# Performance work log

Measured on AMD Instinct MI355X. Metric: run time of the kernel, lower is better.

## Reference

```python
import jax, jax.numpy as jnp
import numpy as np

N = 100000
E = 1600000
G = 2048          # number of graphs in the batch
HEADS = 4
HID = 16          # per-head channels
IN_CH = 128
D = HEADS * HID   # 64, concat output width per layer
NEG_SLOPE = 0.2


def _gat_layer(x, src, dst, W, a_src, a_dst, bias):
    # x: [N, Fin], W: [Fin, H*C], a_src/a_dst: [H, C], bias: [H*C]
    h = (x @ W).reshape(N, HEADS, HID)                      # [N, H, C]
    al_s = jnp.einsum('nhc,hc->nh', h, a_src)               # [N, H]
    al_d = jnp.einsum('nhc,hc->nh', h, a_dst)               # [N, H]
    e = jax.nn.leaky_relu(al_s[src] + al_d[dst], NEG_SLOPE) # [E+N, H]
    # segment softmax over incoming edges of each destination node
    m = jax.ops.segment_max(e, dst, num_segments=N)         # [N, H]
    e = jnp.exp(e - m[dst])
    s = jax.ops.segment_sum(e, dst, num_segments=N)
    alpha = e / (s[dst] + 1e-16)                            # [E+N, H]
    msg = h[src] * alpha[..., None]                         # [E+N, H, C]
    out = jax.ops.segment_sum(msg, dst, num_segments=N)     # [N, H, C]
    return out.reshape(N, D) + bias


def setup_inputs() -> dict:
    key = jax.random.key(0)
    ks = jax.random.split(key, 16)
    x = jax.random.normal(ks[0], (N, IN_CH), dtype=jnp.float32)
    edge_index = jax.random.randint(ks[1], (2, E), 0, N, dtype=jnp.int64)
    batch = jnp.sort(jax.random.randint(ks[2], (N,), 0, G, dtype=jnp.int64))
    inp = {'x': x, 'edge_index': edge_index, 'batch': batch}
    fins = [IN_CH, D, D]
    for i, fin in enumerate(fins):
        kk = jax.random.split(ks[3 + i], 4)
        sc = 1.0 / np.sqrt(fin)
        inp[f'W{i}'] = jax.random.normal(kk[0], (fin, D), dtype=jnp.float32) * sc
        inp[f'as{i}'] = jax.random.normal(kk[1], (HEADS, HID), dtype=jnp.float32) * 0.1
        inp[f'ad{i}'] = jax.random.normal(kk[2], (HEADS, HID), dtype=jnp.float32) * 0.1
        inp[f'b{i}'] = jnp.zeros((D,), dtype=jnp.float32)
    inp['head_w'] = jax.random.normal(ks[10], (1, D), dtype=jnp.float32) * (1.0 / np.sqrt(D))
    inp['head_b'] = jnp.zeros((1,), dtype=jnp.float32)
    return inp


def reference(x, edge_index, batch,
              W0, as0, ad0, b0,
              W1, as1, ad1, b1,
              W2, as2, ad2, b2,
              head_w, head_b):
    # PyG GATConv adds self-loops by default
    loops = jnp.arange(N, dtype=edge_index.dtype)
    src = jnp.concatenate([edge_index[0], loops])
    dst = jnp.concatenate([edge_index[1], loops])
    layers = [(W0, as0, ad0, b0), (W1, as1, ad1, b1), (W2, as2, ad2, b2)]
    h = x.astype(jnp.float32)
    for (W, a_s, a_d, b) in layers:
        h = _gat_layer(h, src, dst, W, a_s, a_d, b)
        h = jax.nn.relu(h)  # dropout p=0.0 -> identity
    pooled = jax.ops.segment_sum(h, batch, num_segments=G)  # [G, D]
    out = pooled @ head_w.T + head_b                         # [G, 1]
    return out.reshape(-1)                                   # out_dim == 1 -> flatten
```

## Files before the change

### kernel.cpp

```cpp
#include <hip/hip_runtime.h>
#include <hip/hip_bf16.h>
#include <hip/hip_fp16.h>
#include <cstdint>
#include <cstddef>

#define NN 100000
#define EE 1600000
#define GG 2048

constexpr int NB_SCAN = (NN + 255) / 256;

typedef __attribute__((ext_vector_type(4))) _Float16 half4v;

__device__ __forceinline__ float lrelu(float v) { return v > 0.f ? v : 0.2f * v; }

__global__ void k_count(const int* __restrict__ ei, int* __restrict__ deg) {
    int i = blockIdx.x * blockDim.x + threadIdx.x;
    if (i >= EE + NN) return;
    int d = (i < EE) ? ei[EE + i] : (i - EE);
    atomicAdd(&deg[d], 1);
}

__global__ void k_scan1(const int* __restrict__ deg, int* __restrict__ offs,
                        int* __restrict__ bsums) {
    __shared__ int tmp[256];
    int tid = threadIdx.x;
    int i = blockIdx.x * 256 + tid;
    int v = (i < NN) ? deg[i] : 0;
    tmp[tid] = v; __syncthreads();
    for (int off = 1; off < 256; off <<= 1) {
        int t = (tid >= off) ? tmp[tid - off] : 0;
        __syncthreads();
        tmp[tid] += t;
        __syncthreads();
    }
    if (i < NN) offs[i] = tmp[tid] - v;
    if (tid == 255) bsums[blockIdx.x] = tmp[255];
}

__global__ void k_scan2(int* __restrict__ bsums) {
    __shared__ int tmp[512];
    int tid = threadIdx.x;
    int v = (tid < NB_SCAN) ? bsums[tid] : 0;
    tmp[tid] = v; __syncthreads();
    for (int off = 1; off < 512; off <<= 1) {
        int t = (tid >= off) ? tmp[tid - off] : 0;
        __syncthreads();
        tmp[tid] += t;
        __syncthreads();
    }
    if (tid < NB_SCAN) bsums[tid] = tmp[tid] - v;
}

__global__ void k_scan3(int* __restrict__ offs, const int* __restrict__ bsums) {
    int i = blockIdx.x * 256 + threadIdx.x;
    if (i < NN) offs[i] += bsums[blockIdx.x];
}

__global__ void k_scatter(const int* __restrict__ ei, const int* __restrict__ offs,
                          int* __restrict__ cursor, int* __restrict__ col) {
    int i = blockIdx.x * blockDim.x + threadIdx.x;
    if (i >= EE + NN) return;
    int s, d;
    if (i < EE) { s = ei[i]; d = ei[EE + i]; } else { s = d = i - EE; }
    int pos = offs[d] + atomicAdd(&cursor[d], 1);
    col[pos] = s;
}

__global__ __launch_bounds__(256) void k_gemm(const float* __restrict__ X,
                                              const float* __restrict__ W,
                                              const float* __restrict__ asrc,
                                              const float* __restrict__ adst,
                                              _Float16* __restrict__ Hh,
                                              float* __restrict__ als,
                                              float* __restrict__ ald, int fin) {
    __shared__ float xs[16 * 128];
    int j  = threadIdx.x & 63;
    int ty = threadIdx.x >> 6;
    int row0 = blockIdx.x * 16;
    int f4 = fin >> 2;
    int lg = (fin == 128) ? 5 : 4;
    const float4* X4 = (const float4*)X;
    int tot4 = 16 * f4;
    for (int idx = threadIdx.x; idx < tot4; idx += 256) {
        int r = idx >> lg, k4 = idx & (f4 - 1);
        ((float4*)xs)[idx] = X4[(size_t)(row0 + r) * f4 + k4];
    }
    __syncthreads();
    const float* x0 = xs + (ty * 4 + 0) * fin;
    const float* x1 = xs + (ty * 4 + 1) * fin;
    const float* x2 = xs + (ty * 4 + 2) * fin;
    const float* x3 = xs + (ty * 4 + 3) * fin;
    float a0 = 0.f, a1 = 0.f, a2 = 0.f, a3 = 0.f;
    for (int k = 0; k < fin; k++) {
        float w = W[k * 64 + j];
        a0 += x0[k] * w; a1 += x1[k] * w; a2 += x2[k] * w; a3 += x3[k] * w;
    }
    int row = row0 + ty * 4;
    Hh[(size_t)(row + 0) * 64 + j] = (_Float16)a0;
    Hh[(size_t)(row + 1) * 64 + j] = (_Float16)a1;
    Hh[(size_t)(row + 2) * 64 + j] = (_Float16)a2;
    Hh[(size_t)(row + 3) * 64 + j] = (_Float16)a3;
    float asj = asrc[j], adj = adst[j];
    float accs[4] = {a0, a1, a2, a3};
#pragma unroll
    for (int r = 0; r < 4; r++) {
        float vs = accs[r] * asj;
        float vd = accs[r] * adj;
#pragma unroll
        for (int off = 8; off > 0; off >>= 1) {
            vs += __shfl_xor(vs, off, 64);
            vd += __shfl_xor(vd, off, 64);
        }
        if ((j & 15) == 0) {
            int h = j >> 4;
            als[(size_t)(row + r) * 4 + h] = vs;
            ald[(size_t)(row + r) * 4 + h] = vd;
        }
    }
}

#define LWPITCH 260
__global__ __launch_bounds__(256) void k_agg(
    const _Float16* __restrict__ Hh, const float* __restrict__ als,
    const float* __restrict__ ald, const int* __restrict__ offs,
    const int* __restrict__ deg, const int* __restrict__ col,
    const float* __restrict__ bias, float* __restrict__ Hout,
    const int* __restrict__ batch, const float* __restrict__ hw,
    float* __restrict__ out, int last) {
    __shared__ float lws[16 * LWPITCH];
    __shared__ int   lsi[16][64];
    int tid = threadIdx.x;
    int g = tid >> 4;
    int l = tid & 15;
    int n = blockIdx.x * 16 + g;
    int start = offs[n];
    int len = deg[n];
    float4 ad4 = ((const float4*)ald)[n];
    int hsel = l >> 2;
    const half4v* Hp = (const half4v*)Hh + l;
    float* lw = lws + g * LWPITCH;
    bool fast = (len <= 64);
    float inv = 1.f;

    if (fast) {
        float ev[4][4];
        int   si[4];
        bool  vld[4];
        float m0 = -1e30f, m1 = -1e30f, m2 = -1e30f, m3 = -1e30f;
#pragma unroll
        for (int it = 0; it < 4; it++) {
            int e = l + it * 16;
            vld[it] = (e < len);
            int s = vld[it] ? col[start + e] : 0;
            si[it] = s;
            float4 a = ((const float4*)als)[s];
            ev[it][0] = lrelu(a.x + ad4.x); ev[it][1] = lrelu(a.y + ad4.y);
            ev[it][2] = lrelu(a.z + ad4.z); ev[it][3] = lrelu(a.w + ad4.w);
            if (vld[it]) {
                m0 = fmaxf(m0, ev[it][0]); m1 = fmaxf(m1, ev[it][1]);
                m2 = fmaxf(m2, ev[it][2]); m3 = fmaxf(m3, ev[it][3]);
            }
        }
#pragma unroll
        for (int off = 8; off > 0; off >>= 1) {
            m0 = fmaxf(m0, __shfl_xor(m0, off, 16));
            m1 = fmaxf(m1, __shfl_xor(m1, off, 16));
            m2 = fmaxf(m2, __shfl_xor(m2, off, 16));
            m3 = fmaxf(m3, __shfl_xor(m3, off, 16));
        }
        float s0 = 0.f, s1 = 0.f, s2 = 0.f, s3 = 0.f;
#pragma unroll
        for (int it = 0; it < 4; it++) {
            int e = l + it * 16;
            float w0 = vld[it] ? __expf(ev[it][0] - m0) : 0.f;
            float w1 = vld[it] ? __expf(ev[it][1] - m1) : 0.f;
            float w2 = vld[it] ? __expf(ev[it][2] - m2) : 0.f;
            float w3 = vld[it] ? __expf(ev[it][3] - m3) : 0.f;
            s0 += w0; s1 += w1; s2 += w2; s3 += w3;
            ((float4*)(lw + e * 4))[0] = make_float4(w0, w1, w2, w3);
            lsi[g][e] = vld[it] ? si[it] : 0;
        }
#pragma unroll
        for (int off = 8; off > 0; off >>= 1) {
            s0 += __shfl_xor(s0, off, 16); s1 += __shfl_xor(s1, off, 16);
            s2 += __shfl_xor(s2, off, 16); s3 += __shfl_xor(s3, off, 16);
        }
        float smh = hsel == 0 ? s0 : hsel == 1 ? s1 : hsel == 2 ? s2 : s3;
        inv = 1.f / (smh + 1e-16f);
    }

    __syncthreads();

    float4 acc = {0.f, 0.f, 0.f, 0.f};
    if (fast) {
        int e = 0;
        for (; e + 4 <= len; e += 4) {
            int sa = lsi[g][e], sb = lsi[g][e + 1], sc = lsi[g][e + 2], sd = lsi[g][e + 3];
            float wa = lw[(e + 0) * 4 + hsel];
            float wb = lw[(e + 1) * 4 + hsel];
            float wc = lw[(e + 2) * 4 + hsel];
            float wd = lw[(e + 3) * 4 + hsel];
            half4v ha = Hp[(size_t)sa * 16];
            half4v hb = Hp[(size_t)sb * 16];
            half4v hc = Hp[(size_t)sc * 16];
            half4v hd = Hp[(size_t)sd * 16];
            acc.x += wa * (float)ha.x + wb * (float)hb.x + wc * (float)hc.x + wd * (float)hd.x;
            acc.y += wa * (float)ha.y + wb * (float)hb.y + wc * (float)hc.y + wd * (float)hd.y;
            acc.z += wa * (float)ha.z + wb * (float)hb.z + wc * (float)hc.z + wd * (float)hd.z;
            acc.w += wa * (float)ha.w + wb * (float)hb.w + wc * (float)hc.w + wd * (float)hd.w;
        }
        for (; e < len; e++) {
            int sa = lsi[g][e];
            float wa = lw[e * 4 + hsel];
            half4v ha = Hp[(size_t)sa * 16];
            acc.x += wa * (float)ha.x; acc.y += wa * (float)ha.y;
            acc.z += wa * (float)ha.z; acc.w += wa * (float)ha.w;
        }
    } else {
        float m0 = -1e30f, m1 = -1e30f, m2 = -1e30f, m3 = -1e30f;
        for (int e = l; e < len; e += 16) {
            int s = col[start + e];
            float4 a = ((const float4*)als)[s];
            m0 = fmaxf(m0, lrelu(a.x + ad4.x)); m1 = fmaxf(m1, lrelu(a.y + ad4.y));
            m2 = fmaxf(m2, lrelu(a.z + ad4.z)); m3 = fmaxf(m3, lrelu(a.w + ad4.w));
        }
#pragma unroll
        for (int off = 8; off > 0; off >>= 1) {
            m0 = fmaxf(m0, __shfl_xor(m0, off, 16));
            m1 = fmaxf(m1, __shfl_xor(m1, off, 16));
            m2 = fmaxf(m2, __shfl_xor(m2, off, 16));
            m3 = fmaxf(m3, __shfl_xor(m3, off, 16));
        }
        float s0 = 0.f, s1 = 0.f, s2 = 0.f, s3 = 0.f;
        for (int e = l; e < len; e += 16) {
            int s = col[start + e];
            float4 a = ((const float4*)als)[s];
            s0 += __expf(lrelu(a.x + ad4.x) - m0); s1 += __expf(lrelu(a.y + ad4.y) - m1);
            s2 += __expf(lrelu(a.z + ad4.z) - m2); s3 += __expf(lrelu(a.w + ad4.w) - m3);
        }
#pragma unroll
        for (int off = 8; off > 0; off >>= 1) {
            s0 += __shfl_xor(s0, off, 16); s1 += __shfl_xor(s1, off, 16);
            s2 += __shfl_xor(s2, off, 16); s3 += __shfl_xor(s3, off, 16);
        }
        float mh = hsel == 0 ? m0 : hsel == 1 ? m1 : hsel == 2 ? m2 : m3;
        float sh = hsel == 0 ? s0 : hsel == 1 ? s1 : hsel == 2 ? s2 : s3;
        float ih = 1.f / (sh + 1e-16f);
        float ah = hsel == 0 ? ad4.x : hsel == 1 ? ad4.y : hsel == 2 ? ad4.z : ad4.w;
        for (int e = 0; e < len; e++) {
            int s = col[start + e];
            float alpha = __expf(lrelu(als[(size_t)s * 4 + hsel] + ah) - mh) * ih;
            half4v ha = Hp[(size_t)s * 16];
            acc.x += alpha * (float)ha.x; acc.y += alpha * (float)ha.y;
            acc.z += alpha * (float)ha.z; acc.w += alpha * (float)ha.w;
        }
        inv = 1.f;
    }

    float4 b4 = ((const float4*)bias)[l];
    float4 o4;
    o4.x = fmaxf(acc.x * inv + b4.x, 0.f);
    o4.y = fmaxf(acc.y * inv + b4.y, 0.f);
    o4.z = fmaxf(acc.z * inv + b4.z, 0.f);
    o4.w = fmaxf(acc.w * inv + b4.w, 0.f);
    if (!last) {
        ((float4*)Hout)[(size_t)n * 16 + l] = o4;
    } else {
        float4 w4 = ((const float4*)hw)[l];
        float t = o4.x * w4.x + o4.y * w4.y + o4.z * w4.z + o4.w * w4.w;
#pragma unroll
        for (int off = 8; off > 0; off >>= 1) t += __shfl_xor(t, off, 16);
        if (l == 0) atomicAdd(&out[batch[n]], t);
    }
}

__global__ void k_out_init(const float* __restrict__ head_b, float* __restrict__ out) {
    int g = blockIdx.x * blockDim.x + threadIdx.x;
    if (g < GG) out[g] = head_b[0];
}

extern "C" void kernel_launch(void* const* d_in, const int* in_sizes, int n_in,
                              void* d_out, int out_size, void* d_ws, size_t ws_size,
                              hipStream_t stream) {
    const float* x     = (const float*)d_in[0];
    const int*   ei    = (const int*)d_in[1];
    const int*   batch = (const int*)d_in[2];
    const float* Wm[3] = {(const float*)d_in[3], (const float*)d_in[7],  (const float*)d_in[11]};
    const float* As[3] = {(const float*)d_in[4], (const float*)d_in[8],  (const float*)d_in[12]};
    const float* Ad[3] = {(const float*)d_in[5], (const float*)d_in[9],  (const float*)d_in[13]};
    const float* Bb[3] = {(const float*)d_in[6], (const float*)d_in[10], (const float*)d_in[14]};
    const float* hw = (const float*)d_in[15];
    const float* hb = (const float*)d_in[16];
    float* out = (float*)d_out;

    uint8_t* w = (uint8_t*)d_ws;
    auto alloc = [&](size_t bytes) -> void* {
        void* p = (void*)w;
        w += (bytes + 255) & ~(size_t)255;
        return p;
    };
    _Float16* Hh   = (_Float16*)alloc((size_t)NN * 64 * 2);
    float* Bf      = (float*)alloc((size_t)NN * 64 * 4);
    float* als     = (float*)alloc((size_t)NN * 4 * 4);
    float* ald     = (float*)alloc((size_t)NN * 4 * 4);
    int*   deg     = (int*)alloc((size_t)NN * 4);
    int*   offs    = (int*)alloc((size_t)NN * 4);
    int*   cursor  = (int*)alloc((size_t)NN * 4);
    int*   col     = (int*)alloc((size_t)(EE + NN) * 4);
    int*   bsums   = (int*)alloc((size_t)((NB_SCAN + 63) & ~63) * 4);

    hipMemsetAsync(deg, 0, (size_t)NN * 4, stream);
    hipMemsetAsync(cursor, 0, (size_t)NN * 4, stream);

    int eb = (EE + NN + 255) / 256;
    k_count  <<<eb, 256, 0, stream>>>(ei, deg);
    k_scan1  <<<NB_SCAN, 256, 0, stream>>>(deg, offs, bsums);
    k_scan2  <<<1, 512, 0, stream>>>(bsums);
    k_scan3  <<<NB_SCAN, 256, 0, stream>>>(offs, bsums);
    k_scatter<<<eb, 256, 0, stream>>>(ei, offs, cursor, col);
    k_out_init<<<(GG + 255) / 256, 256, 0, stream>>>(hb, out);

    const float* cur_in = x;
    int fin = 128;
    for (int L = 0; L < 3; L++) {
        k_gemm<<<NN / 16, 256, 0, stream>>>(
            cur_in, Wm[L], As[L], Ad[L], Hh, als, ald, fin);
        k_agg <<<NN / 16, 256, 0, stream>>>(
            Hh, als, ald, offs, deg, col, Bb[L], Bf, batch, hw, out, (L == 2) ? 1 : 0);
        cur_in = Bf;
        fin = 64;
    }
}
```

Baseline: 648.0 us.

## Store features in fp32, reuse atomic ranks for CSR scatter, templatize GEMM

Three separate changes. The atomic rank from the degree count is recorded per edge and reused in the scatter, which removes the second atomic pass and the cursor memset. The GEMM is templated on input width and reads X directly with float4 loads, dropping the shared-memory staging. The projected features are also stored in fp32 instead of fp16, which doubles the bytes gathered per edge in aggregation in exchange for avoiding conversions and precision loss.

```diff
diff --git a/kernel.cpp b/kernel.cpp
--- a/kernel.cpp
+++ b/kernel.cpp
@@ -10,15 +10,14 @@
 
 constexpr int NB_SCAN = (NN + 255) / 256;
 
-typedef __attribute__((ext_vector_type(4))) _Float16 half4v;
-
 __device__ __forceinline__ float lrelu(float v) { return v > 0.f ? v : 0.2f * v; }
 
-__global__ void k_count(const int* __restrict__ ei, int* __restrict__ deg) {
+__global__ void k_count(const int* __restrict__ ei, int* __restrict__ deg,
+                        int* __restrict__ rank) {
     int i = blockIdx.x * blockDim.x + threadIdx.x;
     if (i >= EE + NN) return;
     int d = (i < EE) ? ei[EE + i] : (i - EE);
-    atomicAdd(&deg[d], 1);
+    rank[i] = atomicAdd(&deg[d], 1);
 }
 
 __global__ void k_scan1(const int* __restrict__ deg, int* __restrict__ offs,
@@ -58,49 +57,49 @@
 }
 
 __global__ void k_scatter(const int* __restrict__ ei, const int* __restrict__ offs,
-                          int* __restrict__ cursor, int* __restrict__ col) {
+                          const int* __restrict__ rank, int* __restrict__ col) {
     int i = blockIdx.x * blockDim.x + threadIdx.x;
     if (i >= EE + NN) return;
     int s, d;
     if (i < EE) { s = ei[i]; d = ei[EE + i]; } else { s = d = i - EE; }
-    int pos = offs[d] + atomicAdd(&cursor[d], 1);
-    col[pos] = s;
-}
-
+    col[offs[d] + rank[i]] = s;
+}
+
+template <int FIN>
 __global__ __launch_bounds__(256) void k_gemm(const float* __restrict__ X,
                                               const float* __restrict__ W,
                                               const float* __restrict__ asrc,
                                               const float* __restrict__ adst,
-                                              _Float16* __restrict__ Hh,
+                                              float* __restrict__ H,
                                               float* __restrict__ als,
-                                              float* __restrict__ ald, int fin) {
-    __shared__ float xs[16 * 128];
+                                              float* __restrict__ ald) {
     int j  = threadIdx.x & 63;
     int ty = threadIdx.x >> 6;
-    int row0 = blockIdx.x * 16;
-    int f4 = fin >> 2;
-    int lg = (fin == 128) ? 5 : 4;
-    const float4* X4 = (const float4*)X;
-    int tot4 = 16 * f4;
-    for (int idx = threadIdx.x; idx < tot4; idx += 256) {
-        int r = idx >> lg, k4 = idx & (f4 - 1);
-        ((float4*)xs)[idx] = X4[(size_t)(row0 + r) * f4 + k4];
-    }
-    __syncthreads();
-    const float* x0 = xs + (ty * 4 + 0) * fin;
-    const float* x1 = xs + (ty * 4 + 1) * fin;
-    const float* x2 = xs + (ty * 4 + 2) * fin;
-    const float* x3 = xs + (ty * 4 + 3) * fin;
+    int row = __builtin_amdgcn_readfirstlane(blockIdx.x * 16 + ty * 4);
+    const float* x0 = X + (size_t)row * FIN;
+    const float* x1 = x0 + FIN;
+    const float* x2 = x1 + FIN;
+    const float* x3 = x2 + FIN;
     float a0 = 0.f, a1 = 0.f, a2 = 0.f, a3 = 0.f;
-    for (int k = 0; k < fin; k++) {
-        float w = W[k * 64 + j];
-        a0 += x0[k] * w; a1 += x1[k] * w; a2 += x2[k] * w; a3 += x3[k] * w;
-    }
-    int row = row0 + ty * 4;
-    Hh[(size_t)(row + 0) * 64 + j] = (_Float16)a0;
-    Hh[(size_t)(row + 1) * 64 + j] = (_Float16)a1;
-    Hh[(size_t)(row + 2) * 64 + j] = (_Float16)a2;
-    Hh[(size_t)(row + 3) * 64 + j] = (_Float16)a3;
+#pragma unroll
+    for (int k = 0; k < FIN; k += 4) {
+        float4 xa = *(const float4*)(x0 + k);
+        float4 xb = *(const float4*)(x1 + k);
+        float4 xc = *(const float4*)(x2 + k);
+        float4 xd = *(const float4*)(x3 + k);
+        float w0 = W[(k + 0) * 64 + j];
+        float w1 = W[(k + 1) * 64 + j];
+        float w2 = W[(k + 2) * 64 + j];
+        float w3 = W[(k + 3) * 64 + j];
+        a0 += xa.x * w0 + xa.y * w1 + xa.z * w2 + xa.w * w3;
+        a1 += xb.x * w0 + xb.y * w1 + xb.z * w2 + xb.w * w3;
+        a2 += xc.x * w0 + xc.y * w1 + xc.z * w2 + xc.w * w3;
+        a3 += xd.x * w0 + xd.y * w1 + xd.z * w2 + xd.w * w3;
+    }
+    H[(size_t)(row + 0) * 64 + j] = a0;
+    H[(size_t)(row + 1) * 64 + j] = a1;
+    H[(size_t)(row + 2) * 64 + j] = a2;
+    H[(size_t)(row + 3) * 64 + j] = a3;
     float asj = asrc[j], adj = adst[j];
     float accs[4] = {a0, a1, a2, a3};
 #pragma unroll
@@ -122,7 +121,7 @@
 
 #define LWPITCH 260
 __global__ __launch_bounds__(256) void k_agg(
-    const _Float16* __restrict__ Hh, const float* __restrict__ als,
+    const float* __restrict__ H, const float* __restrict__ als,
     const float* __restrict__ ald, const int* __restrict__ offs,
     const int* __restrict__ deg, const int* __restrict__ col,
     const float* __restrict__ bias, float* __restrict__ Hout,
@@ -138,7 +137,7 @@
     int len = deg[n];
     float4 ad4 = ((const float4*)ald)[n];
     int hsel = l >> 2;
-    const half4v* Hp = (const half4v*)Hh + l;
+    const float4* Hp = (const float4*)H + l;
     float* lw = lws + g * LWPITCH;
     bool fast = (len <= 64);
     float inv = 1.f;
@@ -201,21 +200,21 @@
             float wb = lw[(e + 1) * 4 + hsel];
             float wc = lw[(e + 2) * 4 + hsel];
             float wd = lw[(e + 3) * 4 + hsel];
-            half4v ha = Hp[(size_t)sa * 16];
-            half4v hb = Hp[(size_t)sb * 16];
-            half4v hc = Hp[(size_t)sc * 16];
-            half4v hd = Hp[(size_t)sd * 16];
-            acc.x += wa * (float)ha.x + wb * (float)hb.x + wc * (float)hc.x + wd * (float)hd.x;
-            acc.y += wa * (float)ha.y + wb * (float)hb.y + wc * (float)hc.y + wd * (float)hd.y;
-            acc.z += wa * (float)ha.z + wb * (float)hb.z + wc * (float)hc.z + wd * (float)hd.z;
-            acc.w += wa * (float)ha.w + wb * (float)hb.w + wc * (float)hc.w + wd * (float)hd.w;
+            float4 ha = Hp[(size_t)sa * 16];
+            float4 hb = Hp[(size_t)sb * 16];
+            float4 hc = Hp[(size_t)sc * 16];
+            float4 hd = Hp[(size_t)sd * 16];
+            acc.x += wa * ha.x + wb * hb.x + wc * hc.x + wd * hd.x;
+            acc.y += wa * ha.y + wb * hb.y + wc * hc.y + wd * hd.y;
+            acc.z += wa * ha.z + wb * hb.z + wc * hc.z + wd * hd.z;
+            acc.w += wa * ha.w + wb * hb.w + wc * hc.w + wd * hd.w;
         }
         for (; e < len; e++) {
             int sa = lsi[g][e];
             float wa = lw[e * 4 + hsel];
-            half4v ha = Hp[(size_t)sa * 16];
-            acc.x += wa * (float)ha.x; acc.y += wa * (float)ha.y;
-            acc.z += wa * (float)ha.z; acc.w += wa * (float)ha.w;
+            float4 ha = Hp[(size_t)sa * 16];
+            acc.x += wa * ha.x; acc.y += wa * ha.y;
+            acc.z += wa * ha.z; acc.w += wa * ha.w;
         }
     } else {
         float m0 = -1e30f, m1 = -1e30f, m2 = -1e30f, m3 = -1e30f;
@@ -251,9 +250,9 @@
         for (int e = 0; e < len; e++) {
             int s = col[start + e];
             float alpha = __expf(lrelu(als[(size_t)s * 4 + hsel] + ah) - mh) * ih;
-            half4v ha = Hp[(size_t)s * 16];
-            acc.x += alpha * (float)ha.x; acc.y += alpha * (float)ha.y;
-            acc.z += alpha * (float)ha.z; acc.w += alpha * (float)ha.w;
+            float4 ha = Hp[(size_t)s * 16];
+            acc.x += alpha * ha.x; acc.y += alpha * ha.y;
+            acc.z += alpha * ha.z; acc.w += alpha * ha.w;
         }
         inv = 1.f;
     }
@@ -300,35 +299,36 @@
         w += (bytes + 255) & ~(size_t)255;
         return p;
     };
-    _Float16* Hh   = (_Float16*)alloc((size_t)NN * 64 * 2);
+    float* H       = (float*)alloc((size_t)NN * 64 * 4);
     float* Bf      = (float*)alloc((size_t)NN * 64 * 4);
     float* als     = (float*)alloc((size_t)NN * 4 * 4);
     float* ald     = (float*)alloc((size_t)NN * 4 * 4);
     int*   deg     = (int*)alloc((size_t)NN * 4);
     int*   offs    = (int*)alloc((size_t)NN * 4);
-    int*   cursor  = (int*)alloc((size_t)NN * 4);
+    int*   rank    = (int*)alloc((size_t)(EE + NN) * 4);
     int*   col     = (int*)alloc((size_t)(EE + NN) * 4);
     int*   bsums   = (int*)alloc((size_t)((NB_SCAN + 63) & ~63) * 4);
 
     hipMemsetAsync(deg, 0, (size_t)NN * 4, stream);
-    hipMemsetAsync(cursor, 0, (size_t)NN * 4, stream);
 
     int eb = (EE + NN + 255) / 256;
-    k_count  <<<eb, 256, 0, stream>>>(ei, deg);
+    k_count  <<<eb, 256, 0, stream>>>(ei, deg, rank);
     k_scan1  <<<NB_SCAN, 256, 0, stream>>>(deg, offs, bsums);
     k_scan2  <<<1, 512, 0, stream>>>(bsums);
     k_scan3  <<<NB_SCAN, 256, 0, stream>>>(offs, bsums);
-    k_scatter<<<eb, 256, 0, stream>>>(ei, offs, cursor, col);
+    k_scatter<<<eb, 256, 0, stream>>>(ei, offs, rank, col);
     k_out_init<<<(GG + 255) / 256, 256, 0, stream>>>(hb, out);
 
     const float* cur_in = x;
-    int fin = 128;
     for (int L = 0; L < 3; L++) {
-        k_gemm<<<NN / 16, 256, 0, stream>>>(
-            cur_in, Wm[L], As[L], Ad[L], Hh, als, ald, fin);
+        if (L == 0)
+            k_gemm<128><<<NN / 16, 256, 0, stream>>>(
+                cur_in, Wm[L], As[L], Ad[L], H, als, ald);
+        else
+            k_gemm<64><<<NN / 16, 256, 0, stream>>>(
+                cur_in, Wm[L], As[L], Ad[L], H, als, ald);
         k_agg <<<NN / 16, 256, 0, stream>>>(
-            Hh, als, ald, offs, deg, col, Bb[L], Bf, batch, hw, out, (L == 2) ? 1 : 0);
+            H, als, ald, offs, deg, col, Bb[L], Bf, batch, hw, out, (L == 2) ? 1 : 0);
         cur_in = Bf;
-        fin = 64;
-    }
-}
+    }
+}
```

Measured after the change: 540.5 us. 1.2x faster.
